# Optimization experiments

Hardware: AMD Instinct MI355X
Metric: run time of the kernel (lower is better)

## Reference

```python
import jax, jax.numpy as jnp
import numpy as np

QUERY_DIM = 192
KEY_DIM = 64
DIM_OUT = 128
C = QUERY_DIM + KEY_DIM  # 256
N = 10000
E = 320000
M = 5000


def setup_inputs() -> dict:
    key = jax.random.key(0)
    ks = jax.random.split(key, 16)
    s = 1.0 / np.sqrt(C)
    inp = {
        "query": jax.random.normal(ks[0], (N, QUERY_DIM), jnp.float32),
        "key_idx": jax.random.randint(ks[1], (N,), 0, KEY_DIM),
        "edge_index": jax.random.randint(ks[2], (2, E), 0, N),
        "mask_idx": jnp.sort(jax.random.randint(ks[3], (M,), 0, N)),
        "Wq": jax.random.normal(ks[4], (C, C), jnp.float32) * s,
        "bq": jnp.zeros((C,), jnp.float32),
        "Wk": jax.random.normal(ks[5], (C, C), jnp.float32) * s,
        "bk": jnp.zeros((C,), jnp.float32),
        "Wv": jax.random.normal(ks[6], (C, C), jnp.float32) * s,
        "bv": jnp.zeros((C,), jnp.float32),
        "Ws": jax.random.normal(ks[7], (C, C), jnp.float32) * s,
        "bs": jnp.zeros((C,), jnp.float32),
        "Wo": jax.random.normal(ks[8], (KEY_DIM, DIM_OUT), jnp.float32) * (1.0 / np.sqrt(KEY_DIM)),
        "bo": jnp.zeros((DIM_OUT,), jnp.float32),
    }
    return inp


def reference(query, key_idx, edge_index, mask_idx, Wq, bq, Wk, bk, Wv, bv, Ws, bs, Wo, bo):
    # node features: [N, C] = concat(query, one_hot(key))
    x = jnp.concatenate([query, jax.nn.one_hot(key_idx, KEY_DIM, dtype=query.dtype)], axis=1)
    src, dst = edge_index[0], edge_index[1]  # messages flow src -> dst
    # node-level projections (dense GEMMs), then edge gather
    q_n = x @ Wq + bq
    k_n = x @ Wk + bk
    v_n = x @ Wv + bv
    q = q_n[dst]  # [E, C]
    k = k_n[src]
    v = v_n[src]
    score = jnp.sum(q * k, axis=-1) / jnp.sqrt(jnp.asarray(C, x.dtype))  # [E]
    # per-destination softmax over incoming edges
    m = jax.ops.segment_max(score, dst, num_segments=N)  # [N]
    m = jnp.where(jnp.isfinite(m), m, 0.0)
    e = jnp.exp(score - m[dst])
    denom = jax.ops.segment_sum(e, dst, num_segments=N)
    alpha = e / (denom[dst] + 1e-16)
    # scatter-aggregate weighted values + root/skip connection
    agg = jax.ops.segment_sum(alpha[:, None] * v, dst, num_segments=N)  # [N, C]
    out = agg + (x @ Ws + bs)
    h = jax.nn.relu(out[mask_idx])  # [M, C]
    h = h[:, QUERY_DIM:]  # [M, KEY_DIM]
    return h @ Wo + bo  # [M, DIM_OUT]
```

## Files before the change

kernel.cpp:

```cpp
#include <hip/hip_runtime.h>

#define QDIM 192
#define KDIM 64
#define CDIM 256
#define DOUT 128
#define CAP 128
#define NEG_INF __int_as_float(0xFF800000)
#define LDP 200

typedef _Float16 hf2 __attribute__((ext_vector_type(2)));
typedef _Float16 half4 __attribute__((ext_vector_type(4)));
typedef _Float16 half8 __attribute__((ext_vector_type(8)));
typedef float floatx4 __attribute__((ext_vector_type(4)));

#if defined(__has_builtin)
#if __has_builtin(__builtin_amdgcn_fdot2)
#define HAVE_FDOT2 1
#endif
#endif

__device__ __forceinline__ hf2 bc_h2(unsigned u) { return __builtin_bit_cast(hf2, u); }

__device__ __forceinline__ float dot2acc(hf2 a, hf2 b, float c) {
#ifdef HAVE_FDOT2
    return __builtin_amdgcn_fdot2(a, b, c, false);
#else
    return c + (float)a[0] * (float)b[0] + (float)a[1] * (float)b[1];
#endif
}

__global__ __launch_bounds__(256) void prep_kernel(
        const float* __restrict__ query, _Float16* __restrict__ Qh,
        int* __restrict__ deg, int qchunks, int N) {
    int t = blockIdx.x * blockDim.x + threadIdx.x;
    if (t < qchunks) {
        float4 v = ((const float4*)query)[t];
        half4 h = { (_Float16)v.x, (_Float16)v.y, (_Float16)v.z, (_Float16)v.w };
        ((half4*)Qh)[t] = h;
        return;
    }
    t -= qchunks;
    if (t < N) deg[t] = (int)0x80000000;
}

__global__ __launch_bounds__(256) void gemm_nodes(
        const _Float16* __restrict__ Qh, const int* __restrict__ key_idx,
        const float* Wq, const float* bq, const float* Wk, const float* bk,
        const float* Wv, const float* bv, const float* Ws, const float* bs,
        const int* __restrict__ mask, int M, int* __restrict__ deg,
        _Float16* __restrict__ Qbuf, _Float16* __restrict__ Kbuf,
        _Float16* __restrict__ Vbuf, float* __restrict__ Sbuf, int N) {
    __shared__ __align__(16) _Float16 As[64 * LDP];
    __shared__ __align__(16) _Float16 Bs[64 * LDP];
    int bm = blockIdx.x * 64;
    int bn = blockIdx.y * 64;
    int tid = threadIdx.x;

    int gid = (blockIdx.y * gridDim.x + blockIdx.x) * 256 + tid;
    if (gid < M) deg[mask[gid]] = 0;

    const float* Wb; const float* bvec; int wc0;
    if (bn < 256)      { Wb = Wq; bvec = bq; wc0 = bn; }
    else if (bn < 512) { Wb = Wk; bvec = bk; wc0 = bn - 256; }
    else if (bn < 576) { Wb = Wv; bvec = bv; wc0 = QDIM + (bn - 512); }
    else               { Wb = Ws; bvec = bs; wc0 = QDIM + (bn - 576); }

    #pragma unroll
    for (int it = 0; it < 6; it++) {
        int idx = tid + it * 256;
        int r = idx / 24, q4 = idx % 24;
        int gr = bm + r;
        uint4 va = make_uint4(0u, 0u, 0u, 0u);
        if (gr < N) va = ((const uint4*)(Qh + (size_t)gr * QDIM))[q4];
        *((uint4*)&As[r * LDP + q4 * 8]) = va;
    }
    {
        int c = tid & 63, r0 = tid >> 6;
        #pragma unroll
        for (int it = 0; it < 6; it++) {
            int kg = r0 + it * 4;
            float f[8];
            #pragma unroll
            for (int j = 0; j < 8; j++)
                f[j] = Wb[(size_t)(kg * 8 + j) * CDIM + wc0 + c];
            half8 h8 = { (_Float16)f[0], (_Float16)f[1], (_Float16)f[2], (_Float16)f[3],
                         (_Float16)f[4], (_Float16)f[5], (_Float16)f[6], (_Float16)f[7] };
            *((half8*)&Bs[c * LDP + kg * 8]) = h8;
        }
    }
    __syncthreads();

    int w = tid >> 6, l = tid & 63;
    int lrow = l & 15, quad = l >> 4;
    floatx4 acc[4] = {{0.f,0.f,0.f,0.f},{0.f,0.f,0.f,0.f},{0.f,0.f,0.f,0.f},{0.f,0.f,0.f,0.f}};

    const _Float16* arow = &As[(w * 16 + lrow) * LDP + quad * 8];
    #pragma unroll
    for (int ks = 0; ks < 6; ks++) {
        half8 af = *(const half8*)(arow + ks * 32);
        #pragma unroll
        for (int nt = 0; nt < 4; nt++) {
            half8 bf = *(const half8*)(&Bs[(nt * 16 + lrow) * LDP + quad * 8 + ks * 32]);
            acc[nt] = __builtin_amdgcn_mfma_f32_16x16x32_f16(af, bf, acc[nt], 0, 0, 0);
        }
    }

    int ki[4];
    #pragma unroll
    for (int reg = 0; reg < 4; reg++) {
        int gr = bm + w * 16 + quad * 4 + reg;
        ki[reg] = (gr < N) ? key_idx[gr] : 0;
    }
    #pragma unroll
    for (int nt = 0; nt < 4; nt++) {
        int gc = bn + nt * 16 + lrow;
        int wc = wc0 + nt * 16 + lrow;
        float bias = bvec[wc];
        #pragma unroll
        for (int reg = 0; reg < 4; reg++) {
            int gr = bm + w * 16 + quad * 4 + reg;
            if (gr < N) {
                float v = acc[nt][reg] + Wb[(size_t)(QDIM + ki[reg]) * CDIM + wc] + bias;
                if (gc < 256)      Qbuf[(size_t)gr * 256 + gc] = (_Float16)v;
                else if (gc < 512) Kbuf[(size_t)gr * 256 + (gc - 256)] = (_Float16)v;
                else if (gc < 576) Vbuf[(size_t)gr * KDIM + (gc - 512)] = (_Float16)v;
                else               Sbuf[(size_t)gr * KDIM + (gc - 576)] = v;
            }
        }
    }
}

__global__ __launch_bounds__(256) void scatter_kernel(
        const int* __restrict__ src, const int* __restrict__ dst,
        int* __restrict__ deg, int* __restrict__ adj, int E) {
    int e = blockIdx.x * blockDim.x + threadIdx.x;
    if (e < E) {
        int d = dst[e];
        int slot = atomicAdd(&deg[d], 1);
        if ((unsigned)slot < CAP) adj[d * CAP + slot] = src[e];
    }
}

__global__ __launch_bounds__(256) void attend_out(
        const _Float16* __restrict__ Qbuf, const _Float16* __restrict__ Kbuf,
        const _Float16* __restrict__ Vbuf, const float* __restrict__ Sbuf,
        const int* __restrict__ deg, const int* __restrict__ adj,
        const int* __restrict__ mask, const float* __restrict__ Wo,
        const float* __restrict__ bo, float* __restrict__ out, int M) {
    int w = threadIdx.x >> 6, lane = threadIdx.x & 63;
    int r = blockIdx.x * 4 + w;
    if (r >= M) return;
    int node = mask[r];
    if (r > 0 && mask[r - 1] == node) return;
    int l = lane & 15, g = lane >> 4;

    const uint4* qp = (const uint4*)(Qbuf + (size_t)node * 256 + l * 16);
    uint4 qa = qp[0], qb = qp[1];
    hf2 qh[8] = { bc_h2(qa.x), bc_h2(qa.y), bc_h2(qa.z), bc_h2(qa.w),
                  bc_h2(qb.x), bc_h2(qb.y), bc_h2(qb.z), bc_h2(qb.w) };

    int dn = min(deg[node], CAP);
    const int* arow = adj + (size_t)node * CAP;

    float m = NEG_INF, dsum = 0.f;
    float a0 = 0.f, a1 = 0.f, a2 = 0.f, a3 = 0.f;
    for (int i = g; i < dn; i += 4) {
        int s = arow[i];
        const uint4* kp = (const uint4*)(Kbuf + (size_t)s * 256 + l * 16);
        uint4 ka = kp[0], kb = kp[1];
        float d = 0.f;
        d = dot2acc(bc_h2(ka.x), qh[0], d);
        d = dot2acc(bc_h2(ka.y), qh[1], d);
        d = dot2acc(bc_h2(ka.z), qh[2], d);
        d = dot2acc(bc_h2(ka.w), qh[3], d);
        d = dot2acc(bc_h2(kb.x), qh[4], d);
        d = dot2acc(bc_h2(kb.y), qh[5], d);
        d = dot2acc(bc_h2(kb.z), qh[6], d);
        d = dot2acc(bc_h2(kb.w), qh[7], d);
        d += __shfl_xor(d, 1, 64);
        d += __shfl_xor(d, 2, 64);
        d += __shfl_xor(d, 4, 64);
        d += __shfl_xor(d, 8, 64);
        float sc = d * 0.0625f;
        float m_new = fmaxf(m, sc);
        float scale = __expf(m - m_new);
        float p = __expf(sc - m_new);
        dsum = dsum * scale + p;
        uint2 vv = *(const uint2*)(Vbuf + (size_t)s * KDIM + l * 4);
        hf2 v01 = bc_h2(vv.x), v23 = bc_h2(vv.y);
        a0 = a0 * scale + p * (float)v01[0];
        a1 = a1 * scale + p * (float)v01[1];
        a2 = a2 * scale + p * (float)v23[0];
        a3 = a3 * scale + p * (float)v23[1];
        m = m_new;
    }

    float Mx = fmaxf(m, __shfl_xor(m, 16, 64));
    Mx = fmaxf(Mx, __shfl_xor(Mx, 32, 64));
    float wgt = (m == NEG_INF) ? 0.f : __expf(m - Mx);
    float ds = dsum * wgt;
    ds += __shfl_xor(ds, 16, 64);
    ds += __shfl_xor(ds, 32, 64);
    a0 *= wgt; a1 *= wgt; a2 *= wgt; a3 *= wgt;
    a0 += __shfl_xor(a0, 16, 64); a0 += __shfl_xor(a0, 32, 64);
    a1 += __shfl_xor(a1, 16, 64); a1 += __shfl_xor(a1, 32, 64);
    a2 += __shfl_xor(a2, 16, 64); a2 += __shfl_xor(a2, 32, 64);
    a3 += __shfl_xor(a3, 16, 64); a3 += __shfl_xor(a3, 32, 64);
    float inv = 1.f / (ds + 1e-16f);

    float4 s4 = *((const float4*)(Sbuf + (size_t)node * KDIM + l * 4));
    float h0 = fmaxf(a0 * inv + s4.x, 0.f);
    float h1 = fmaxf(a1 * inv + s4.y, 0.f);
    float h2 = fmaxf(a2 * inv + s4.z, 0.f);
    float h3 = fmaxf(a3 * inv + s4.w, 0.f);

    float o0 = bo[lane], o1 = bo[lane + 64];
    #pragma unroll
    for (int c = 0; c < KDIM; c++) {
        float hc = (c & 3) == 0 ? h0 : (c & 3) == 1 ? h1 : (c & 3) == 2 ? h2 : h3;
        float hv = __shfl(hc, c >> 2, 64);
        o0 += hv * Wo[c * DOUT + lane];
        o1 += hv * Wo[c * DOUT + 64 + lane];
    }
    int rr = r;
    do {
        out[(size_t)rr * DOUT + lane] = o0;
        out[(size_t)rr * DOUT + 64 + lane] = o1;
        rr++;
    } while (rr < M && mask[rr] == node);
}

extern "C" void kernel_launch(void* const* d_in, const int* in_sizes, int n_in,
                              void* d_out, int out_size, void* d_ws, size_t ws_size,
                              hipStream_t stream) {
    const float* query    = (const float*)d_in[0];
    const int* key_idx    = (const int*)d_in[1];
    const int* edge_index = (const int*)d_in[2];
    const int* mask_idx   = (const int*)d_in[3];
    const float* Wq = (const float*)d_in[4];
    const float* bq = (const float*)d_in[5];
    const float* Wk = (const float*)d_in[6];
    const float* bk = (const float*)d_in[7];
    const float* Wv = (const float*)d_in[8];
    const float* bv = (const float*)d_in[9];
    const float* Ws = (const float*)d_in[10];
    const float* bs = (const float*)d_in[11];
    const float* Wo = (const float*)d_in[12];
    const float* bo = (const float*)d_in[13];

    int N = in_sizes[0] / QDIM;
    int E = in_sizes[2] / 2;
    int M = in_sizes[3];
    const int* esrc = edge_index;
    const int* edst = edge_index + E;

    char* wsb = (char*)d_ws;
    size_t off = 0;
    auto alloc = [&](size_t nbytes) { char* p = wsb + off; off += (nbytes + 15) & ~15ull; return p; };
    _Float16* Qh   = (_Float16*)alloc((size_t)N * QDIM * 2);
    _Float16* Qbuf = (_Float16*)alloc((size_t)N * 256 * 2);
    _Float16* Kbuf = (_Float16*)alloc((size_t)N * 256 * 2);
    _Float16* Vbuf = (_Float16*)alloc((size_t)N * KDIM * 2);
    float* Sbuf    = (float*)alloc((size_t)N * KDIM * 4);
    int*   deg     = (int*)alloc((size_t)N * 4);
    int*   adj     = (int*)alloc((size_t)N * CAP * 4);

    int qchunks = N * QDIM / 4;
    prep_kernel<<<(qchunks + N + 255) / 256, 256, 0, stream>>>(query, Qh, deg, qchunks, N);

    dim3 ggrid((N + 63) / 64, 10);
    gemm_nodes<<<ggrid, 256, 0, stream>>>(Qh, key_idx, Wq, bq, Wk, bk, Wv, bv,
                                          Ws, bs, mask_idx, M, deg,
                                          Qbuf, Kbuf, Vbuf, Sbuf, N);

    scatter_kernel<<<(E + 255) / 256, 256, 0, stream>>>(esrc, edst, deg, adj, E);

    attend_out<<<(M + 3) / 4, 256, 0, stream>>>(Qbuf, Kbuf, Vbuf, Sbuf, deg, adj,
                                                mask_idx, Wo, bo, (float*)d_out, M);
}
```

Baseline: 149.4 us.

## Pre-transpose weights, fuse edge scatter into GEMM, prefetch neighbors in attention

The prep kernel now converts and transposes the weight columns to fp16 once and precomputes the one-hot rows plus bias. It also marks masked nodes in deg with a binary search over the sorted mask. The GEMM loads B tiles with coalesced vector reads and does the edge scatter in a grid-stride loop, which removes the separate scatter launch. The attention loop software-prefetches the next neighbor's K/V rows and index to hide gather latency. The costs are one extra prep pass over the weights and higher register use in the attention loop.

```diff
diff --git a/kernel.cpp b/kernel.cpp
--- a/kernel.cpp
+++ b/kernel.cpp
@@ -5,6 +5,7 @@
 #define CDIM 256
 #define DOUT 128
 #define CAP 128
+#define NVCOL 640
 #define NEG_INF __int_as_float(0xFF800000)
 #define LDP 200
 
@@ -31,6 +32,12 @@
 
 __global__ __launch_bounds__(256) void prep_kernel(
         const float* __restrict__ query, _Float16* __restrict__ Qh,
+        const float* __restrict__ Wq, const float* __restrict__ bq,
+        const float* __restrict__ Wk, const float* __restrict__ bk,
+        const float* __restrict__ Wv, const float* __restrict__ bv,
+        const float* __restrict__ Ws, const float* __restrict__ bs,
+        const int* __restrict__ mask, int M,
+        _Float16* __restrict__ WhT, float* __restrict__ OB,
         int* __restrict__ deg, int qchunks, int N) {
     int t = blockIdx.x * blockDim.x + threadIdx.x;
     if (t < qchunks) {
@@ -40,14 +47,41 @@
         return;
     }
     t -= qchunks;
-    if (t < N) deg[t] = (int)0x80000000;
+    if (t < NVCOL * QDIM) {
+        int v = t / QDIM, r = t - v * QDIM;
+        const float* Wseg; int col;
+        if (v < 256)      { Wseg = Wq; col = v; }
+        else if (v < 512) { Wseg = Wk; col = v - 256; }
+        else if (v < 576) { Wseg = Wv; col = QDIM + (v - 512); }
+        else              { Wseg = Ws; col = QDIM + (v - 576); }
+        WhT[t] = (_Float16)Wseg[(size_t)r * CDIM + col];
+        return;
+    }
+    t -= NVCOL * QDIM;
+    if (t < NVCOL * KDIM) {
+        int v = t >> 6, kidx = t & 63;
+        const float* Wseg; const float* bseg; int col;
+        if (v < 256)      { Wseg = Wq; bseg = bq; col = v; }
+        else if (v < 512) { Wseg = Wk; bseg = bk; col = v - 256; }
+        else if (v < 576) { Wseg = Wv; bseg = bv; col = QDIM + (v - 512); }
+        else              { Wseg = Ws; bseg = bs; col = QDIM + (v - 576); }
+        OB[t] = Wseg[(size_t)(QDIM + kidx) * CDIM + col] + bseg[col];
+        return;
+    }
+    t -= NVCOL * KDIM;
+    if (t < N) {
+        int lo = 0, hi = M;
+        while (lo < hi) { int mid = (lo + hi) >> 1; if (mask[mid] < t) lo = mid + 1; else hi = mid; }
+        bool found = (lo < M) && (mask[lo] == t);
+        deg[t] = found ? 0 : (int)0x80000000;
+    }
 }
 
 __global__ __launch_bounds__(256) void gemm_nodes(
         const _Float16* __restrict__ Qh, const int* __restrict__ key_idx,
-        const float* Wq, const float* bq, const float* Wk, const float* bk,
-        const float* Wv, const float* bv, const float* Ws, const float* bs,
-        const int* __restrict__ mask, int M, int* __restrict__ deg,
+        const _Float16* __restrict__ WhT, const float* __restrict__ OB,
+        const int* __restrict__ esrc, const int* __restrict__ edst,
+        int* __restrict__ deg, int* __restrict__ adj, int E,
         _Float16* __restrict__ Qbuf, _Float16* __restrict__ Kbuf,
         _Float16* __restrict__ Vbuf, float* __restrict__ Sbuf, int N) {
     __shared__ __align__(16) _Float16 As[64 * LDP];
@@ -56,14 +90,12 @@
     int bn = blockIdx.y * 64;
     int tid = threadIdx.x;
 
-    int gid = (blockIdx.y * gridDim.x + blockIdx.x) * 256 + tid;
-    if (gid < M) deg[mask[gid]] = 0;
-
-    const float* Wb; const float* bvec; int wc0;
-    if (bn < 256)      { Wb = Wq; bvec = bq; wc0 = bn; }
-    else if (bn < 512) { Wb = Wk; bvec = bk; wc0 = bn - 256; }
-    else if (bn < 576) { Wb = Wv; bvec = bv; wc0 = QDIM + (bn - 512); }
-    else               { Wb = Ws; bvec = bs; wc0 = QDIM + (bn - 576); }
+    int total = gridDim.x * gridDim.y * 256;
+    for (int e = (blockIdx.y * gridDim.x + blockIdx.x) * 256 + tid; e < E; e += total) {
+        int d = edst[e];
+        int slot = atomicAdd(&deg[d], 1);
+        if ((unsigned)slot < CAP) adj[(size_t)d * CAP + slot] = esrc[e];
+    }
 
     #pragma unroll
     for (int it = 0; it < 6; it++) {
@@ -74,19 +106,12 @@
         if (gr < N) va = ((const uint4*)(Qh + (size_t)gr * QDIM))[q4];
         *((uint4*)&As[r * LDP + q4 * 8]) = va;
     }
-    {
-        int c = tid & 63, r0 = tid >> 6;
-        #pragma unroll
-        for (int it = 0; it < 6; it++) {
-            int kg = r0 + it * 4;
-            float f[8];
-            #pragma unroll
-            for (int j = 0; j < 8; j++)
-                f[j] = Wb[(size_t)(kg * 8 + j) * CDIM + wc0 + c];
-            half8 h8 = { (_Float16)f[0], (_Float16)f[1], (_Float16)f[2], (_Float16)f[3],
-                         (_Float16)f[4], (_Float16)f[5], (_Float16)f[6], (_Float16)f[7] };
-            *((half8*)&Bs[c * LDP + kg * 8]) = h8;
-        }
+    #pragma unroll
+    for (int it = 0; it < 6; it++) {
+        int idx = tid + it * 256;
+        int cc = idx / 24, q4 = idx % 24;
+        uint4 vb = ((const uint4*)(WhT + (size_t)(bn + cc) * QDIM))[q4];
+        *((uint4*)&Bs[cc * LDP + q4 * 8]) = vb;
     }
     __syncthreads();
 
@@ -114,30 +139,18 @@
     #pragma unroll
     for (int nt = 0; nt < 4; nt++) {
         int gc = bn + nt * 16 + lrow;
-        int wc = wc0 + nt * 16 + lrow;
-        float bias = bvec[wc];
+        const float* obc = OB + (size_t)gc * KDIM;
         #pragma unroll
         for (int reg = 0; reg < 4; reg++) {
             int gr = bm + w * 16 + quad * 4 + reg;
             if (gr < N) {
-                float v = acc[nt][reg] + Wb[(size_t)(QDIM + ki[reg]) * CDIM + wc] + bias;
+                float v = acc[nt][reg] + obc[ki[reg]];
                 if (gc < 256)      Qbuf[(size_t)gr * 256 + gc] = (_Float16)v;
                 else if (gc < 512) Kbuf[(size_t)gr * 256 + (gc - 256)] = (_Float16)v;
                 else if (gc < 576) Vbuf[(size_t)gr * KDIM + (gc - 512)] = (_Float16)v;
                 else               Sbuf[(size_t)gr * KDIM + (gc - 576)] = v;
             }
         }
-    }
-}
-
-__global__ __launch_bounds__(256) void scatter_kernel(
-        const int* __restrict__ src, const int* __restrict__ dst,
-        int* __restrict__ deg, int* __restrict__ adj, int E) {
-    int e = blockIdx.x * blockDim.x + threadIdx.x;
-    if (e < E) {
-        int d = dst[e];
-        int slot = atomicAdd(&deg[d], 1);
-        if ((unsigned)slot < CAP) adj[d * CAP + slot] = src[e];
     }
 }
 
@@ -164,10 +177,21 @@
 
     float m = NEG_INF, dsum = 0.f;
     float a0 = 0.f, a1 = 0.f, a2 = 0.f, a3 = 0.f;
+
+    uint4 ka, kb; uint2 vv; int s_nxt = 0;
+    if (dn > 0) {
+        int s0 = arow[min(g, dn - 1)];
+        const uint4* kp = (const uint4*)(Kbuf + (size_t)s0 * 256 + l * 16);
+        ka = kp[0]; kb = kp[1];
+        vv = *(const uint2*)(Vbuf + (size_t)s0 * KDIM + l * 4);
+        s_nxt = arow[min(g + 4, dn - 1)];
+    }
     for (int i = g; i < dn; i += 4) {
-        int s = arow[i];
-        const uint4* kp = (const uint4*)(Kbuf + (size_t)s * 256 + l * 16);
-        uint4 ka = kp[0], kb = kp[1];
+        const uint4* kp2 = (const uint4*)(Kbuf + (size_t)s_nxt * 256 + l * 16);
+        uint4 ka2 = kp2[0], kb2 = kp2[1];
+        uint2 vv2 = *(const uint2*)(Vbuf + (size_t)s_nxt * KDIM + l * 4);
+        int s_aft = arow[min(i + 8, dn - 1)];
+
         float d = 0.f;
         d = dot2acc(bc_h2(ka.x), qh[0], d);
         d = dot2acc(bc_h2(ka.y), qh[1], d);
@@ -186,13 +210,13 @@
         float scale = __expf(m - m_new);
         float p = __expf(sc - m_new);
         dsum = dsum * scale + p;
-        uint2 vv = *(const uint2*)(Vbuf + (size_t)s * KDIM + l * 4);
         hf2 v01 = bc_h2(vv.x), v23 = bc_h2(vv.y);
         a0 = a0 * scale + p * (float)v01[0];
         a1 = a1 * scale + p * (float)v01[1];
         a2 = a2 * scale + p * (float)v23[0];
         a3 = a3 * scale + p * (float)v23[1];
         m = m_new;
+        ka = ka2; kb = kb2; vv = vv2; s_nxt = s_aft;
     }
 
     float Mx = fmaxf(m, __shfl_xor(m, 16, 64));
@@ -258,6 +282,8 @@
     size_t off = 0;
     auto alloc = [&](size_t nbytes) { char* p = wsb + off; off += (nbytes + 15) & ~15ull; return p; };
     _Float16* Qh   = (_Float16*)alloc((size_t)N * QDIM * 2);
+    _Float16* WhT  = (_Float16*)alloc((size_t)NVCOL * QDIM * 2);
+    float* OB      = (float*)alloc((size_t)NVCOL * KDIM * 4);
     _Float16* Qbuf = (_Float16*)alloc((size_t)N * 256 * 2);
     _Float16* Kbuf = (_Float16*)alloc((size_t)N * 256 * 2);
     _Float16* Vbuf = (_Float16*)alloc((size_t)N * KDIM * 2);
@@ -266,14 +292,13 @@
     int*   adj     = (int*)alloc((size_t)N * CAP * 4);
 
     int qchunks = N * QDIM / 4;
-    prep_kernel<<<(qchunks + N + 255) / 256, 256, 0, stream>>>(query, Qh, deg, qchunks, N);
+    int total1 = qchunks + NVCOL * QDIM + NVCOL * KDIM + N;
+    prep_kernel<<<(total1 + 255) / 256, 256, 0, stream>>>(
+        query, Qh, Wq, bq, Wk, bk, Wv, bv, Ws, bs, mask_idx, M, WhT, OB, deg, qchunks, N);
 
     dim3 ggrid((N + 63) / 64, 10);
-    gemm_nodes<<<ggrid, 256, 0, stream>>>(Qh, key_idx, Wq, bq, Wk, bk, Wv, bv,
-                                          Ws, bs, mask_idx, M, deg,
+    gemm_nodes<<<ggrid, 256, 0, stream>>>(Qh, key_idx, WhT, OB, esrc, edst, deg, adj, E,
                                           Qbuf, Kbuf, Vbuf, Sbuf, N);
-
-    scatter_kernel<<<(E + 255) / 256, 256, 0, stream>>>(esrc, edst, deg, adj, E);
 
     attend_out<<<(M + 3) / 4, 256, 0, stream>>>(Qbuf, Kbuf, Vbuf, Sbuf, deg, adj,
                                                 mask_idx, Wo, bo, (float*)d_out, M);
```

Result: no change. 149.1 us (-0.2%).
